# Kernel optimization log

Hardware: AMD Instinct MI355X
Metric: run time of the kernel (lower is better)

## Reference

```python
import jax, jax.numpy as jnp
import numpy as np

ID_LENGTH = 4   # number of identity images cached in the id bank
HEADS = 20      # SDXL attention heads at channel 1280
SA32 = 0.5


def setup_inputs() -> dict:
    key = jax.random.key(0)
    ks = jax.random.split(key, 7)
    B2, T, C = 8, 576, 1280            # 2*id_length images, 576 tokens each (768/32)^2
    S = ID_LENGTH * T                   # 2304 grouped sequence length
    hidden_states = jax.random.normal(ks[0], (B2, T, C), jnp.float32)
    # cal_attn_mask_xl: one random row pattern repeated, with each image's own
    # block forced True (sliced to the [:id_length*T, :id_length*T] write-mode mask)
    row_pat = jax.random.uniform(ks[1], (1, S)) < SA32
    mask = jnp.tile(row_pat, (S, 1))
    img = jnp.arange(S) // T
    mask = mask | (img[:, None] == img[None, :])
    w = lambda k: jax.random.normal(k, (C, C), jnp.float32) * 0.02
    return {
        "hidden_states": hidden_states,
        "mask": mask,
        "Wq": w(ks[2]), "Wk": w(ks[3]), "Wv": w(ks[4]), "Wo": w(ks[5]),
        "bo": jnp.zeros((C,), jnp.float32),
    }


def reference(hidden_states, mask, Wq, Wk, Wv, Wo, bo):
    # __call1__ path: regroup [2*id_length, T, C] -> [2, id_length*T, C]
    B2, T, C = hidden_states.shape
    hs = hidden_states.reshape(2, ID_LENGTH * T, C)
    hd = C // HEADS

    def split_heads(x):  # [2, S, C] -> [2, H, S, hd]
        return x.reshape(2, -1, HEADS, hd).transpose(0, 2, 1, 3)

    q = split_heads(hs @ Wq)
    k = split_heads(hs @ Wk)   # write mode: encoder_hidden_states == hidden_states
    v = split_heads(hs @ Wv)

    scores = jnp.einsum('bhqd,bhkd->bhqk', q, k) / jnp.sqrt(jnp.asarray(hd, q.dtype))
    scores = jnp.where(mask[None, None], scores, jnp.finfo(scores.dtype).min)
    attnw = jax.nn.softmax(scores, axis=-1)
    out = jnp.einsum('bhqk,bhkd->bhqd', attnw, v)
    out = out.transpose(0, 2, 1, 3).reshape(2, -1, C)
    out = out @ Wo + bo                 # attn.to_out[0]
    return out.reshape(B2, T, C)
```

## Files before the change

### kernel.cpp

```cpp
#include <hip/hip_runtime.h>
#include <hip/hip_bf16.h>
#include <stdint.h>
#include <math.h>

#define S_TOT 2304
#define C_DIM 1280
#define NHEAD 20
#define HD    64
#define M_TOT 4608
#define BH_STRIDE (S_TOT * HD)
#define SC_ROWS 2624
#define KC_STRIDE (SC_ROWS * 64)
#define LOG2E 1.44269504088896f
#define C_SC  (0.125f * LOG2E)
#define MFIX  12.0f
#define QBLK  192

typedef __attribute__((ext_vector_type(8))) short bf16x8;
typedef __attribute__((ext_vector_type(4))) float f32x4;

__device__ __forceinline__ short f2bf(float f) {
    union { float f; uint32_t u; } v; v.f = f;
    uint32_t r = v.u + 0x7FFFu + ((v.u >> 16) & 1u);
    return (short)(r >> 16);
}

__device__ __forceinline__ uint32_t pack2bf(float a, float b) {
    __hip_bfloat162 h = __float22bfloat162_rn(make_float2(a, b));
    union { __hip_bfloat162 h; uint32_t u; } cv; cv.h = h; return cv.u;
}

__device__ __forceinline__ f32x4 zero4() {
    f32x4 z; z[0] = 0.f; z[1] = 0.f; z[2] = 0.f; z[3] = 0.f; return z;
}

__device__ __forceinline__ void gload_lds16(const void* g, void* l) {
    __builtin_amdgcn_global_load_lds(
        (const __attribute__((address_space(1))) uint32_t*)g,
        (__attribute__((address_space(3))) uint32_t*)l, 16, 0, 0);
}

__global__ __launch_bounds__(256)
void prologue(const float* __restrict__ hs, short* __restrict__ hsb,
              const float* __restrict__ W0, const float* __restrict__ W1,
              const float* __restrict__ W2, const float* __restrict__ W3,
              short* __restrict__ T0, short* __restrict__ T1,
              short* __restrict__ T2, short* __restrict__ T3,
              const int* __restrict__ mask, int* __restrict__ hdr,
              int* __restrict__ destmap) {
    __shared__ float tile[32][33];
    __shared__ unsigned long long wbits[36];
    __shared__ int pp[36], dd[36], hb[9];

    const int bx = blockIdx.x;
    const int t = threadIdx.x;

    if (bx < 2880) {
        const int i = bx * 256 + t;
        const float4 v0 = reinterpret_cast<const float4*>(hs)[i * 2];
        const float4 v1 = reinterpret_cast<const float4*>(hs)[i * 2 + 1];
        bf16x8 o;
        o[0] = f2bf(v0.x); o[1] = f2bf(v0.y); o[2] = f2bf(v0.z); o[3] = f2bf(v0.w);
        o[4] = f2bf(v1.x); o[5] = f2bf(v1.y); o[6] = f2bf(v1.z); o[7] = f2bf(v1.w);
        reinterpret_cast<bf16x8*>(hsb)[i] = o;
    } else if (bx < 9280) {
        int id = bx - 2880;
        const int z = id / 1600; id -= z * 1600;
        const int by = id / 40, bxx = id - by * 40;
        const float* W; short* T;
        switch (z) {
            case 0:  W = W0; T = T0; break;
            case 1:  W = W1; T = T1; break;
            case 2:  W = W2; T = T2; break;
            default: W = W3; T = T3; break;
        }
        const int tx = t & 31, ty = t >> 5;
        const int k0 = by * 32, n0 = bxx * 32;
#pragma unroll
        for (int i = 0; i < 4; ++i)
            tile[ty + i * 8][tx] = W[(size_t)(k0 + ty + i * 8) * C_DIM + n0 + tx];
        __syncthreads();
#pragma unroll
        for (int i = 0; i < 4; ++i)
            T[(size_t)(n0 + ty + i * 8) * C_DIM + k0 + tx] = f2bf(tile[tx][ty + i * 8]);
    } else {
        for (int it = 0; it < 9; ++it) {
            const int k = it * 256 + t;
            const int src = (k < 1152) ? 1152 : 0;
            const bool pat = mask[(size_t)src * S_TOT + k] != 0;
            unsigned long long b = __ballot(pat);
            if ((t & 63) == 0) wbits[it * 4 + (t >> 6)] = b;
        }
        __syncthreads();
        if (t == 0) {
            int pcum = 0, dcum[4] = {0, 0, 0, 0};
            for (int wdx = 0; wdx < 36; ++wdx) {
                const int img = wdx / 9;
                const int pc = __popcll(wbits[wdx]);
                pp[wdx] = pcum; dd[wdx] = dcum[img];
                pcum += pc; dcum[img] += 64 - pc;
            }
            hb[0] = pcum;
            int base = (pcum + 63) & ~63;
            for (int i = 0; i < 4; ++i) {
                hb[1 + i] = base; hb[5 + i] = dcum[i];
                base += (dcum[i] + 63) & ~63;
            }
            for (int i = 0; i < 9; ++i) hdr[i] = hb[i];
        }
        __syncthreads();
        if (t < 36) {
            const unsigned long long w64 = wbits[t];
            const int img = t / 9;
            const int pbase = pp[t], dbase = hb[1 + img] + dd[t];
            int pc = 0, dc = 0;
            for (int b = 0; b < 64; ++b) {
                if ((w64 >> b) & 1) destmap[t * 64 + b] = pbase + (pc++);
                else                destmap[t * 64 + b] = dbase + (dc++);
            }
        }
    }
}

__global__ __launch_bounds__(256)
void zero_pads(const int* __restrict__ hdr, short* __restrict__ Kc,
               short* __restrict__ Vr) {
    const int bh = blockIdx.x;
    const int t = threadIdx.x;
    short* Kb = Kc + (size_t)bh * KC_STRIDE;
    short* Vb = Vr + (size_t)bh * KC_STRIDE;
    for (int seg = 0; seg < 5; ++seg) {
        const int cnt = (seg == 0) ? hdr[0] : hdr[4 + seg];
        const int sb  = (seg == 0) ? 0      : hdr[seg];
        const int s0 = sb + cnt;
        const int nrows = ((cnt + 63) & ~63) - cnt;
        for (int idx = t; idx < nrows * 64; idx += 256) {
            const int r = idx >> 6, d = idx & 63;
            Kb[(size_t)(s0 + r) * 64 + d] = 0;
            Vb[(size_t)(s0 + r) * 64 + d] = 0;
        }
    }
}

__global__ __launch_bounds__(256)
void transp_v(const short* __restrict__ Vr, short* __restrict__ Vc) {
    __shared__ short tile[64][72];
    const int bh = blockIdx.y;
    const int s0 = blockIdx.x * 64;
    const int t = threadIdx.x;
    const short* src = Vr + (size_t)bh * KC_STRIDE;
    short* dst = Vc + (size_t)bh * KC_STRIDE;

#pragma unroll
    for (int i = 0; i < 2; ++i) {
        const int e = (i * 256 + t) * 8;
        const int r = e >> 6, c = e & 63;
        bf16x8 v = *(const bf16x8*)(src + (size_t)(s0 + r) * 64 + c);
        *(bf16x8*)&tile[r][c] = v;
    }
    __syncthreads();
    const int d = t & 63, c0 = (t >> 6) * 16;
    short tmp[16];
#pragma unroll
    for (int j = 0; j < 16; ++j) tmp[j] = tile[c0 + j][d];
    *(bf16x8*)(dst + (size_t)d * SC_ROWS + s0 + c0) = *(const bf16x8*)tmp;
    *(bf16x8*)(dst + (size_t)d * SC_ROWS + s0 + c0 + 8) = *(const bf16x8*)(tmp + 8);
}

__global__ __launch_bounds__(256, 2)
void gemm_qkv3(const short* __restrict__ hsb,
               const short* __restrict__ Wtq, const short* __restrict__ Wtk,
               const short* __restrict__ Wtv, const int* __restrict__ destmap,
               short* __restrict__ Qb, short* __restrict__ Kc, short* __restrict__ Vr) {
    __shared__ short As[128 * 64];
    __shared__ short Bs[3 * 128 * 64];
    __shared__ int dm[128];

    const int bid = blockIdx.x;
    const int vid = (bid & 7) * 45 + (bid >> 3);
    const int n0 = (vid / 36) * 128, m0 = (vid % 36) * 128;
    const int t = threadIdx.x;
    const int lane = t & 63, w = t >> 6;
    const int g = lane >> 4, l15 = lane & 15;
    const int wm = w >> 1, wn = w & 1;

    if (t < 128) {
        const int s0 = (m0 >= S_TOT) ? m0 - S_TOT : m0;
        dm[t] = destmap[s0 + t];
    }

    f32x4 acc[3][4][4];
#pragma unroll
    for (int z = 0; z < 3; ++z)
#pragma unroll
        for (int mi = 0; mi < 4; ++mi)
#pragma unroll
            for (int ni = 0; ni < 4; ++ni) acc[z][mi][ni] = zero4();

    for (int k0 = 0; k0 < C_DIM; k0 += 64) {
        __syncthreads();
#pragma unroll
        for (int i = 0; i < 4; ++i) {
            const int F = i * 4096 + t * 16;
            const int row = F >> 7;
            const int colb = (F & 127) ^ ((row & 7) << 4);
            gload_lds16((const char*)hsb + ((size_t)(m0 + row) * C_DIM + k0) * 2 + colb,
                        (char*)As + F);
        }
#pragma unroll
        for (int z = 0; z < 3; ++z) {
            const short* Wt = (z == 0) ? Wtq : (z == 1) ? Wtk : Wtv;
#pragma unroll
            for (int i = 0; i < 4; ++i) {
                const int F = i * 4096 + t * 16;
                const int row = F >> 7;
                const int colb = (F & 127) ^ ((row & 7) << 4);
                gload_lds16((const char*)Wt + ((size_t)(n0 + row) * C_DIM + k0) * 2 + colb,
                            (char*)Bs + z * 16384 + F);
            }
        }
        __syncthreads();

#pragma unroll
        for (int ks = 0; ks < 2; ++ks) {
            const int kb = ks * 64 + g * 16;
            bf16x8 af[4];
#pragma unroll
            for (int mi = 0; mi < 4; ++mi) {
                const int row = wm * 64 + mi * 16 + l15;
                af[mi] = *(const bf16x8*)((const char*)As + row * 128 + (kb ^ ((row & 7) << 4)));
            }
#pragma unroll
            for (int z = 0; z < 3; ++z) {
                bf16x8 bfr[4];
#pragma unroll
                for (int ni = 0; ni < 4; ++ni) {
                    const int row = wn * 64 + ni * 16 + l15;
                    bfr[ni] = *(const bf16x8*)((const char*)Bs + z * 16384 + row * 128 + (kb ^ ((row & 7) << 4)));
                }
                __builtin_amdgcn_s_setprio(1);
#pragma unroll
                for (int mi = 0; mi < 4; ++mi)
#pragma unroll
                    for (int ni = 0; ni < 4; ++ni)
                        acc[z][mi][ni] = __builtin_amdgcn_mfma_f32_16x16x32_bf16(
                            af[mi], bfr[ni], acc[z][mi][ni], 0, 0, 0);
                __builtin_amdgcn_s_setprio(0);
            }
        }
    }

#pragma unroll
    for (int z = 0; z < 3; ++z)
#pragma unroll
        for (int mi = 0; mi < 4; ++mi)
#pragma unroll
            for (int ni = 0; ni < 4; ++ni)
#pragma unroll
                for (int r = 0; r < 4; ++r) {
                    const int m = m0 + wm * 64 + mi * 16 + g * 4 + r;
                    const int n = n0 + wn * 64 + ni * 16 + l15;
                    const int bg = (m >= S_TOT) ? 1 : 0;
                    const int s = m - bg * S_TOT;
                    const int h = n >> 6, d = n & 63;
                    const size_t bh = (size_t)(bg * NHEAD + h);
                    float aval = acc[z][mi][ni][r];
                    if (z == 0) aval *= C_SC;
                    const short v = f2bf(aval);
                    if (z == 0) {
                        Qb[bh * BH_STRIDE + (size_t)s * HD + d] = v;
                    } else {
                        const int sc = dm[m - m0];
                        short* dst = (z == 1) ? Kc : Vr;
                        dst[bh * (size_t)KC_STRIDE + (size_t)sc * 64 + d] = v;
                    }
                }
}

__device__ __forceinline__ void gemm_core(const short* __restrict__ A,
                                          const short* __restrict__ Wt,
                                          int m0, int n0,
                                          f32x4 acc[4][4],
                                          short* AsB, short* BsB) {
    const int t = threadIdx.x;
    const int lane = t & 63, w = t >> 6;
    const int g = lane >> 4, l15 = lane & 15;
    const int wm = w >> 1, wn = w & 1;

#pragma unroll
    for (int mi = 0; mi < 4; ++mi)
#pragma unroll
        for (int ni = 0; ni < 4; ++ni) acc[mi][ni] = zero4();

    auto stage = [&](int k0, int buf) {
#pragma unroll
        for (int i = 0; i < 4; ++i) {
            const int F = i * 4096 + t * 16;
            const int row = F >> 7;
            const int b = F & 127;
            const int colb = b ^ ((row & 7) << 4);
            gload_lds16((const char*)A + ((size_t)(m0 + row) * C_DIM + k0) * 2 + colb,
                        (char*)AsB + buf * 16384 + F);
            gload_lds16((const char*)Wt + ((size_t)(n0 + row) * C_DIM + k0) * 2 + colb,
                        (char*)BsB + buf * 16384 + F);
        }
    };

    stage(0, 0);
    asm volatile("s_waitcnt vmcnt(0)" ::: "memory");
    __builtin_amdgcn_s_barrier();
    __builtin_amdgcn_sched_barrier(0);

    int cur = 0;
    for (int k0 = 0; k0 < C_DIM; k0 += 64) {
        if (k0 + 64 < C_DIM) stage(k0 + 64, cur ^ 1);
        const char* Ac = (const char*)AsB + cur * 16384;
        const char* Bc = (const char*)BsB + cur * 16384;
#pragma unroll
        for (int ks = 0; ks < 2; ++ks) {
            const int kb = ks * 64 + g * 16;
            bf16x8 af[4], bfr[4];
#pragma unroll
            for (int mi = 0; mi < 4; ++mi) {
                const int row = wm * 64 + mi * 16 + l15;
                af[mi] = *(const bf16x8*)(Ac + row * 128 + (kb ^ ((row & 7) << 4)));
            }
#pragma unroll
            for (int ni = 0; ni < 4; ++ni) {
                const int row = wn * 64 + ni * 16 + l15;
                bfr[ni] = *(const bf16x8*)(Bc + row * 128 + (kb ^ ((row & 7) << 4)));
            }
            __builtin_amdgcn_s_setprio(1);
#pragma unroll
            for (int mi = 0; mi < 4; ++mi)
#pragma unroll
                for (int ni = 0; ni < 4; ++ni)
                    acc[mi][ni] = __builtin_amdgcn_mfma_f32_16x16x32_bf16(
                        af[mi], bfr[ni], acc[mi][ni], 0, 0, 0);
            __builtin_amdgcn_s_setprio(0);
        }
        asm volatile("s_waitcnt vmcnt(0)" ::: "memory");
        __builtin_amdgcn_s_barrier();
        __builtin_amdgcn_sched_barrier(0);
        cur ^= 1;
    }
}

__global__ __launch_bounds__(256)
void gemm_out(const short* __restrict__ Ab, const short* __restrict__ Wto,
              const float* __restrict__ bo, float* __restrict__ out) {
    __shared__ short As[2 * 128 * 64];
    __shared__ short Bs[2 * 128 * 64];
    const int bid = blockIdx.x;
    const int vid = (bid & 7) * 45 + (bid >> 3);
    const int n0 = (vid / 36) * 128, m0 = (vid % 36) * 128;

    f32x4 acc[4][4];
    gemm_core(Ab, Wto, m0, n0, acc, As, Bs);

    const int t = threadIdx.x;
    const int lane = t & 63, w = t >> 6, g = lane >> 4, l15 = lane & 15;
    const int wm = w >> 1, wn = w & 1;
#pragma unroll
    for (int mi = 0; mi < 4; ++mi)
#pragma unroll
        for (int ni = 0; ni < 4; ++ni) {
            const int n = n0 + wn * 64 + ni * 16 + l15;
            const float bias = bo[n];
#pragma unroll
            for (int r = 0; r < 4; ++r) {
                const int m = m0 + wm * 64 + mi * 16 + g * 4 + r;
                out[(size_t)m * C_DIM + n] = acc[mi][ni][r] + bias;
            }
        }
}

__global__ __launch_bounds__(768)
void attn_mfma(const short* __restrict__ Qb, const short* __restrict__ Kc,
               const short* __restrict__ Vc, const int* __restrict__ hdr,
               short* __restrict__ Ab) {
    __shared__ short Ks[3][4096];
    __shared__ short Vs[3][4096];
    __shared__ short Ps[QBLK * 64];

    const int t = threadIdx.x;
    const int lane = t & 63, w = t >> 6, g = lane >> 4, l15 = lane & 15;
    const int bid = blockIdx.x;
    const int vid = (bid & 7) * 60 + (bid >> 3);
    const int bh_i = vid / 12, qb = vid % 12;
    const int b = bh_i / NHEAD, h = bh_i % NHEAD;
    const int q0 = qb * QBLK;
    const size_t bh = (size_t)bh_i;
    const int qimg = qb / 3;

    const int cntp  = hdr[0];
    const int dbase = hdr[1 + qimg];
    const int cntd  = hdr[5 + qimg];
    const int ntp = (cntp + 63) >> 6, ntd = (cntd + 63) >> 6, nt = ntp + ntd;

    const short* Qp = Qb + bh * BH_STRIDE;
    const short* Kp = Kc + bh * (size_t)KC_STRIDE;
    const short* Vp = Vc + bh * (size_t)KC_STRIDE;

    bf16x8 qf[2];
    {
        const int row = q0 + w * 16 + l15;
        qf[0] = *(const bf16x8*)(Qp + (size_t)row * HD + g * 8);
        qf[1] = *(const bf16x8*)(Qp + (size_t)row * HD + 32 + g * 8);
    }

    bf16x8 onesv;
#pragma unroll
    for (int j = 0; j < 8; ++j) onesv[j] = (short)0x3F80;

    const f32x4 sinit = {-MFIX, -MFIX, -MFIX, -MFIX};
    f32x4 o_acc[4], lacc;
#pragma unroll
    for (int df = 0; df < 4; ++df) o_acc[df] = zero4();
    lacc = zero4();

    const int rowP = w * 16 + l15;
    const int swzP = (rowP & 7) << 4;
    const int ckbase = g * 4;

    auto tstart = [&](int tt) {
        return (tt < ntp) ? tt * 64 : dbase + (tt - ntp) * 64;
    };
    auto stage = [&](int start, int bufsel) {
        if (t < 512) {
            const int F = t * 16;
            const int row = F >> 7, bb = F & 127;
            const int colb = bb ^ ((row & 7) << 4);
            gload_lds16((const char*)Kp + (size_t)(start + row) * 128 + colb,
                        (char*)Ks[bufsel] + F);
            gload_lds16((const char*)Vp + (size_t)row * (SC_ROWS * 2) + start * 2 + colb,
                        (char*)Vs[bufsel] + F);
        }
    };

    stage(tstart(0), 0);
    if (nt > 1) stage(tstart(1), 1);
    asm volatile("s_waitcnt vmcnt(2)" ::: "memory");
    __builtin_amdgcn_s_barrier();
    __builtin_amdgcn_sched_barrier(0);

    for (int tt = 0; tt < nt; ++tt) {
        const int cur = tt % 3;
        if (tt + 2 < nt) stage(tstart(tt + 2), (tt + 2) % 3);
        const int lim = (tt < ntp) ? cntp - tt * 64 : cntd - (tt - ntp) * 64;

        f32x4 sacc[4];
#pragma unroll
        for (int nf = 0; nf < 4; ++nf) sacc[nf] = sinit;
        __builtin_amdgcn_s_setprio(1);
#pragma unroll
        for (int ks = 0; ks < 2; ++ks) {
            const int kb = ks * 64 + g * 16;
#pragma unroll
            for (int nf = 0; nf < 4; ++nf) {
                const int row = nf * 16 + l15;
                bf16x8 kf = *(const bf16x8*)((const char*)Ks[cur] + row * 128 + (kb ^ ((row & 7) << 4)));
                sacc[nf] = __builtin_amdgcn_mfma_f32_16x16x32_bf16(kf, qf[ks], sacc[nf], 0, 0, 0);
            }
        }
        __builtin_amdgcn_s_setprio(0);

        if (lim < 64) {
#pragma unroll
            for (int nf = 0; nf < 4; ++nf)
#pragma unroll
                for (int r = 0; r < 4; ++r)
                    if (nf * 16 + ckbase + r >= lim) sacc[nf][r] = -1e30f;
        }

#pragma unroll
        for (int nf = 0; nf < 4; ++nf) {
            uint2 u;
            u.x = pack2bf(__builtin_amdgcn_exp2f(sacc[nf][0]),
                          __builtin_amdgcn_exp2f(sacc[nf][1]));
            u.y = pack2bf(__builtin_amdgcn_exp2f(sacc[nf][2]),
                          __builtin_amdgcn_exp2f(sacc[nf][3]));
            *(uint2*)((char*)Ps + rowP * 128 + ((nf * 32 + g * 8) ^ swzP)) = u;
        }

        __builtin_amdgcn_s_setprio(1);
#pragma unroll
        for (int ks = 0; ks < 2; ++ks) {
            const int kb = ks * 64 + g * 16;
            bf16x8 pf = *(const bf16x8*)((const char*)Ps + rowP * 128 + (kb ^ swzP));
            lacc = __builtin_amdgcn_mfma_f32_16x16x32_bf16(onesv, pf, lacc, 0, 0, 0);
#pragma unroll
            for (int df = 0; df < 4; ++df) {
                const int rowV = df * 16 + l15;
                bf16x8 vf = *(const bf16x8*)((const char*)Vs[cur] + rowV * 128 + (kb ^ ((rowV & 7) << 4)));
                o_acc[df] = __builtin_amdgcn_mfma_f32_16x16x32_bf16(vf, pf, o_acc[df], 0, 0, 0);
            }
        }
        __builtin_amdgcn_s_setprio(0);

        asm volatile("s_waitcnt vmcnt(2)" ::: "memory");
        __builtin_amdgcn_s_barrier();
        __builtin_amdgcn_sched_barrier(0);
    }

    const float inv = 1.f / lacc[0];
    const int rowg = b * S_TOT + q0 + w * 16 + l15;
#pragma unroll
    for (int df = 0; df < 4; ++df) {
        uint2 u;
        u.x = pack2bf(o_acc[df][0] * inv, o_acc[df][1] * inv);
        u.y = pack2bf(o_acc[df][2] * inv, o_acc[df][3] * inv);
        *(uint2*)(Ab + (size_t)rowg * C_DIM + h * 64 + df * 16 + g * 4) = u;
    }
}

extern "C" void kernel_launch(void* const* d_in, const int* in_sizes, int n_in,
                              void* d_out, int out_size, void* d_ws, size_t ws_size,
                              hipStream_t stream)
{
    const float* hs   = (const float*)d_in[0];
    const int*   mask = (const int*)  d_in[1];
    const float* Wq   = (const float*)d_in[2];
    const float* Wk   = (const float*)d_in[3];
    const float* Wv   = (const float*)d_in[4];
    const float* Wo   = (const float*)d_in[5];
    const float* bo   = (const float*)d_in[6];
    float* out = (float*)d_out;

    char* ws = (char*)d_ws;
    const size_t mat_b = (size_t)M_TOT * C_DIM * 2;
    const size_t w_b   = (size_t)C_DIM * C_DIM * 2;
    const size_t kc_b  = (size_t)40 * KC_STRIDE * 2;

    short* hsb = (short*)ws;                 ws += mat_b;
    short* Wtq = (short*)ws;                 ws += w_b;
    short* Wtk = (short*)ws;                 ws += w_b;
    short* Wtv = (short*)ws;                 ws += w_b;
    short* Wto = (short*)ws;                 ws += w_b;
    short* Qb  = (short*)ws;                 ws += mat_b;
    short* Kc  = (short*)ws;                 ws += kc_b;
    short* Vr  = (short*)ws;                 ws += kc_b;
    short* Vc  = (short*)ws;                 ws += kc_b;
    short* Ab  = (short*)ws;                 ws += mat_b;
    int*   hdr = (int*)ws;                   ws += 64;
    int*   destmap = (int*)ws;               ws += S_TOT * 4;

    prologue<<<9281, 256, 0, stream>>>(hs, hsb, Wq, Wk, Wv, Wo,
                                       Wtq, Wtk, Wtv, Wto, mask, hdr, destmap);
    zero_pads<<<40, 256, 0, stream>>>(hdr, Kc, Vr);

    gemm_qkv3<<<360, 256, 0, stream>>>(
        hsb, Wtq, Wtk, Wtv, destmap, Qb, Kc, Vr);

    transp_v<<<dim3(SC_ROWS / 64, 40), 256, 0, stream>>>(Vr, Vc);

    attn_mfma<<<480, 768, 0, stream>>>(Qb, Kc, Vc, hdr, Ab);

    gemm_out<<<360, 256, 0, stream>>>(Ab, Wto, bo, out);
}
```

Baseline: 169.3 us.

## Give each attention wave three query fragments and widen output GEMM tile

The attention kernel drops from 12 waves per block to 4 waves, each handling 48 query rows in three 16-row fragments. Every K and V fragment read from LDS is reused across three MFMAs, which cuts LDS traffic per unit of compute at the cost of more registers and lower occupancy. The output GEMM moves to 256x128 tiles with 512 threads and 180 blocks, replacing the double-buffered async pipeline with single-buffered loads bracketed by __syncthreads. Losing the load/compute overlap in that GEMM may expose global memory latency.

```diff
diff --git a/kernel.cpp b/kernel.cpp
--- a/kernel.cpp
+++ b/kernel.cpp
@@ -277,45 +277,48 @@
                 }
 }
 
-__device__ __forceinline__ void gemm_core(const short* __restrict__ A,
-                                          const short* __restrict__ Wt,
-                                          int m0, int n0,
-                                          f32x4 acc[4][4],
-                                          short* AsB, short* BsB) {
+__global__ __launch_bounds__(512)
+void gemm_out(const short* __restrict__ Ab, const short* __restrict__ Wto,
+              const float* __restrict__ bo, float* __restrict__ out) {
+    __shared__ short As[256 * 64];
+    __shared__ short Bs[128 * 64];
+
+    const int bid = blockIdx.x;
+    const int xcd = bid & 7, idx = bid >> 3;
+    const int vid = (xcd < 4) ? xcd * 23 + idx : 92 + (xcd - 4) * 22 + idx;
+    const int m0 = (vid % 18) * 256, n0 = (vid / 18) * 128;
+
     const int t = threadIdx.x;
     const int lane = t & 63, w = t >> 6;
     const int g = lane >> 4, l15 = lane & 15;
     const int wm = w >> 1, wn = w & 1;
 
+    f32x4 acc[4][4];
 #pragma unroll
     for (int mi = 0; mi < 4; ++mi)
 #pragma unroll
         for (int ni = 0; ni < 4; ++ni) acc[mi][ni] = zero4();
 
-    auto stage = [&](int k0, int buf) {
+    for (int k0 = 0; k0 < C_DIM; k0 += 64) {
+        __syncthreads();
 #pragma unroll
         for (int i = 0; i < 4; ++i) {
-            const int F = i * 4096 + t * 16;
+            const int F = i * 8192 + t * 16;
             const int row = F >> 7;
-            const int b = F & 127;
-            const int colb = b ^ ((row & 7) << 4);
-            gload_lds16((const char*)A + ((size_t)(m0 + row) * C_DIM + k0) * 2 + colb,
-                        (char*)AsB + buf * 16384 + F);
-            gload_lds16((const char*)Wt + ((size_t)(n0 + row) * C_DIM + k0) * 2 + colb,
-                        (char*)BsB + buf * 16384 + F);
-        }
-    };
-
-    stage(0, 0);
-    asm volatile("s_waitcnt vmcnt(0)" ::: "memory");
-    __builtin_amdgcn_s_barrier();
-    __builtin_amdgcn_sched_barrier(0);
-
-    int cur = 0;
-    for (int k0 = 0; k0 < C_DIM; k0 += 64) {
-        if (k0 + 64 < C_DIM) stage(k0 + 64, cur ^ 1);
-        const char* Ac = (const char*)AsB + cur * 16384;
-        const char* Bc = (const char*)BsB + cur * 16384;
+            const int colb = (F & 127) ^ ((row & 7) << 4);
+            gload_lds16((const char*)Ab + ((size_t)(m0 + row) * C_DIM + k0) * 2 + colb,
+                        (char*)As + F);
+        }
+#pragma unroll
+        for (int i = 0; i < 2; ++i) {
+            const int F = i * 8192 + t * 16;
+            const int row = F >> 7;
+            const int colb = (F & 127) ^ ((row & 7) << 4);
+            gload_lds16((const char*)Wto + ((size_t)(n0 + row) * C_DIM + k0) * 2 + colb,
+                        (char*)Bs + F);
+        }
+        __syncthreads();
+
 #pragma unroll
         for (int ks = 0; ks < 2; ++ks) {
             const int kb = ks * 64 + g * 16;
@@ -323,12 +326,12 @@
 #pragma unroll
             for (int mi = 0; mi < 4; ++mi) {
                 const int row = wm * 64 + mi * 16 + l15;
-                af[mi] = *(const bf16x8*)(Ac + row * 128 + (kb ^ ((row & 7) << 4)));
+                af[mi] = *(const bf16x8*)((const char*)As + row * 128 + (kb ^ ((row & 7) << 4)));
             }
 #pragma unroll
             for (int ni = 0; ni < 4; ++ni) {
                 const int row = wn * 64 + ni * 16 + l15;
-                bfr[ni] = *(const bf16x8*)(Bc + row * 128 + (kb ^ ((row & 7) << 4)));
+                bfr[ni] = *(const bf16x8*)((const char*)Bs + row * 128 + (kb ^ ((row & 7) << 4)));
             }
             __builtin_amdgcn_s_setprio(1);
 #pragma unroll
@@ -339,28 +342,8 @@
                         af[mi], bfr[ni], acc[mi][ni], 0, 0, 0);
             __builtin_amdgcn_s_setprio(0);
         }
-        asm volatile("s_waitcnt vmcnt(0)" ::: "memory");
-        __builtin_amdgcn_s_barrier();
-        __builtin_amdgcn_sched_barrier(0);
-        cur ^= 1;
-    }
-}
-
-__global__ __launch_bounds__(256)
-void gemm_out(const short* __restrict__ Ab, const short* __restrict__ Wto,
-              const float* __restrict__ bo, float* __restrict__ out) {
-    __shared__ short As[2 * 128 * 64];
-    __shared__ short Bs[2 * 128 * 64];
-    const int bid = blockIdx.x;
-    const int vid = (bid & 7) * 45 + (bid >> 3);
-    const int n0 = (vid / 36) * 128, m0 = (vid % 36) * 128;
-
-    f32x4 acc[4][4];
-    gemm_core(Ab, Wto, m0, n0, acc, As, Bs);
-
-    const int t = threadIdx.x;
-    const int lane = t & 63, w = t >> 6, g = lane >> 4, l15 = lane & 15;
-    const int wm = w >> 1, wn = w & 1;
+    }
+
 #pragma unroll
     for (int mi = 0; mi < 4; ++mi)
 #pragma unroll
@@ -375,7 +358,7 @@
         }
 }
 
-__global__ __launch_bounds__(768)
+__global__ __launch_bounds__(256, 2)
 void attn_mfma(const short* __restrict__ Qb, const short* __restrict__ Kc,
                const short* __restrict__ Vc, const int* __restrict__ hdr,
                short* __restrict__ Ab) {
@@ -402,11 +385,12 @@
     const short* Kp = Kc + bh * (size_t)KC_STRIDE;
     const short* Vp = Vc + bh * (size_t)KC_STRIDE;
 
-    bf16x8 qf[2];
-    {
-        const int row = q0 + w * 16 + l15;
-        qf[0] = *(const bf16x8*)(Qp + (size_t)row * HD + g * 8);
-        qf[1] = *(const bf16x8*)(Qp + (size_t)row * HD + 32 + g * 8);
+    bf16x8 qf[3][2];
+#pragma unroll
+    for (int f = 0; f < 3; ++f) {
+        const int row = q0 + w * 48 + f * 16 + l15;
+        qf[f][0] = *(const bf16x8*)(Qp + (size_t)row * HD + g * 8);
+        qf[f][1] = *(const bf16x8*)(Qp + (size_t)row * HD + 32 + g * 8);
     }
 
     bf16x8 onesv;
@@ -414,21 +398,21 @@
     for (int j = 0; j < 8; ++j) onesv[j] = (short)0x3F80;
 
     const f32x4 sinit = {-MFIX, -MFIX, -MFIX, -MFIX};
-    f32x4 o_acc[4], lacc;
-#pragma unroll
-    for (int df = 0; df < 4; ++df) o_acc[df] = zero4();
-    lacc = zero4();
-
-    const int rowP = w * 16 + l15;
-    const int swzP = (rowP & 7) << 4;
-    const int ckbase = g * 4;
+    f32x4 o_acc[3][4], lacc[3];
+#pragma unroll
+    for (int f = 0; f < 3; ++f) {
+        lacc[f] = zero4();
+#pragma unroll
+        for (int df = 0; df < 4; ++df) o_acc[f][df] = zero4();
+    }
 
     auto tstart = [&](int tt) {
         return (tt < ntp) ? tt * 64 : dbase + (tt - ntp) * 64;
     };
     auto stage = [&](int start, int bufsel) {
-        if (t < 512) {
-            const int F = t * 16;
+#pragma unroll
+        for (int i = 0; i < 2; ++i) {
+            const int F = i * 4096 + t * 16;
             const int row = F >> 7, bb = F & 127;
             const int colb = bb ^ ((row & 7) << 4);
             gload_lds16((const char*)Kp + (size_t)(start + row) * 128 + colb,
@@ -440,18 +424,21 @@
 
     stage(tstart(0), 0);
     if (nt > 1) stage(tstart(1), 1);
-    asm volatile("s_waitcnt vmcnt(2)" ::: "memory");
+    asm volatile("s_waitcnt vmcnt(4)" ::: "memory");
     __builtin_amdgcn_s_barrier();
     __builtin_amdgcn_sched_barrier(0);
 
     for (int tt = 0; tt < nt; ++tt) {
         const int cur = tt % 3;
-        if (tt + 2 < nt) stage(tstart(tt + 2), (tt + 2) % 3);
+        const bool pre = (tt + 2 < nt);
+        if (pre) stage(tstart(tt + 2), (tt + 2) % 3);
         const int lim = (tt < ntp) ? cntp - tt * 64 : cntd - (tt - ntp) * 64;
 
-        f32x4 sacc[4];
-#pragma unroll
-        for (int nf = 0; nf < 4; ++nf) sacc[nf] = sinit;
+        f32x4 sacc[3][4];
+#pragma unroll
+        for (int f = 0; f < 3; ++f)
+#pragma unroll
+            for (int nf = 0; nf < 4; ++nf) sacc[f][nf] = sinit;
         __builtin_amdgcn_s_setprio(1);
 #pragma unroll
         for (int ks = 0; ks < 2; ++ks) {
@@ -460,57 +447,79 @@
             for (int nf = 0; nf < 4; ++nf) {
                 const int row = nf * 16 + l15;
                 bf16x8 kf = *(const bf16x8*)((const char*)Ks[cur] + row * 128 + (kb ^ ((row & 7) << 4)));
-                sacc[nf] = __builtin_amdgcn_mfma_f32_16x16x32_bf16(kf, qf[ks], sacc[nf], 0, 0, 0);
+#pragma unroll
+                for (int f = 0; f < 3; ++f)
+                    sacc[f][nf] = __builtin_amdgcn_mfma_f32_16x16x32_bf16(kf, qf[f][ks], sacc[f][nf], 0, 0, 0);
             }
         }
         __builtin_amdgcn_s_setprio(0);
 
         if (lim < 64) {
 #pragma unroll
-            for (int nf = 0; nf < 4; ++nf)
-#pragma unroll
-                for (int r = 0; r < 4; ++r)
-                    if (nf * 16 + ckbase + r >= lim) sacc[nf][r] = -1e30f;
-        }
-
-#pragma unroll
-        for (int nf = 0; nf < 4; ++nf) {
-            uint2 u;
-            u.x = pack2bf(__builtin_amdgcn_exp2f(sacc[nf][0]),
-                          __builtin_amdgcn_exp2f(sacc[nf][1]));
-            u.y = pack2bf(__builtin_amdgcn_exp2f(sacc[nf][2]),
-                          __builtin_amdgcn_exp2f(sacc[nf][3]));
-            *(uint2*)((char*)Ps + rowP * 128 + ((nf * 32 + g * 8) ^ swzP)) = u;
+            for (int f = 0; f < 3; ++f)
+#pragma unroll
+                for (int nf = 0; nf < 4; ++nf)
+#pragma unroll
+                    for (int r = 0; r < 4; ++r)
+                        if (nf * 16 + g * 4 + r >= lim) sacc[f][nf][r] = -1e30f;
+        }
+
+#pragma unroll
+        for (int f = 0; f < 3; ++f) {
+            const int rowP = w * 48 + f * 16 + l15;
+            const int swzP = (rowP & 7) << 4;
+#pragma unroll
+            for (int nf = 0; nf < 4; ++nf) {
+                uint2 u;
+                u.x = pack2bf(__builtin_amdgcn_exp2f(sacc[f][nf][0]),
+                              __builtin_amdgcn_exp2f(sacc[f][nf][1]));
+                u.y = pack2bf(__builtin_amdgcn_exp2f(sacc[f][nf][2]),
+                              __builtin_amdgcn_exp2f(sacc[f][nf][3]));
+                *(uint2*)((char*)Ps + rowP * 128 + ((nf * 32 + g * 8) ^ swzP)) = u;
+            }
         }
 
         __builtin_amdgcn_s_setprio(1);
 #pragma unroll
         for (int ks = 0; ks < 2; ++ks) {
             const int kb = ks * 64 + g * 16;
-            bf16x8 pf = *(const bf16x8*)((const char*)Ps + rowP * 128 + (kb ^ swzP));
-            lacc = __builtin_amdgcn_mfma_f32_16x16x32_bf16(onesv, pf, lacc, 0, 0, 0);
+            bf16x8 pf[3];
+#pragma unroll
+            for (int f = 0; f < 3; ++f) {
+                const int rowP = w * 48 + f * 16 + l15;
+                pf[f] = *(const bf16x8*)((const char*)Ps + rowP * 128 + (kb ^ ((rowP & 7) << 4)));
+            }
+#pragma unroll
+            for (int f = 0; f < 3; ++f)
+                lacc[f] = __builtin_amdgcn_mfma_f32_16x16x32_bf16(onesv, pf[f], lacc[f], 0, 0, 0);
 #pragma unroll
             for (int df = 0; df < 4; ++df) {
                 const int rowV = df * 16 + l15;
                 bf16x8 vf = *(const bf16x8*)((const char*)Vs[cur] + rowV * 128 + (kb ^ ((rowV & 7) << 4)));
-                o_acc[df] = __builtin_amdgcn_mfma_f32_16x16x32_bf16(vf, pf, o_acc[df], 0, 0, 0);
+#pragma unroll
+                for (int f = 0; f < 3; ++f)
+                    o_acc[f][df] = __builtin_amdgcn_mfma_f32_16x16x32_bf16(vf, pf[f], o_acc[f][df], 0, 0, 0);
             }
         }
         __builtin_amdgcn_s_setprio(0);
 
-        asm volatile("s_waitcnt vmcnt(2)" ::: "memory");
+        if (pre) { asm volatile("s_waitcnt vmcnt(4)" ::: "memory"); }
+        else     { asm volatile("s_waitcnt vmcnt(0)" ::: "memory"); }
         __builtin_amdgcn_s_barrier();
         __builtin_amdgcn_sched_barrier(0);
     }
 
-    const float inv = 1.f / lacc[0];
-    const int rowg = b * S_TOT + q0 + w * 16 + l15;
-#pragma unroll
-    for (int df = 0; df < 4; ++df) {
-        uint2 u;
-        u.x = pack2bf(o_acc[df][0] * inv, o_acc[df][1] * inv);
-        u.y = pack2bf(o_acc[df][2] * inv, o_acc[df][3] * inv);
-        *(uint2*)(Ab + (size_t)rowg * C_DIM + h * 64 + df * 16 + g * 4) = u;
+#pragma unroll
+    for (int f = 0; f < 3; ++f) {
+        const float inv = 1.f / lacc[f][0];
+        const int rowg = b * S_TOT + q0 + w * 48 + f * 16 + l15;
+#pragma unroll
+        for (int df = 0; df < 4; ++df) {
+            uint2 u;
+            u.x = pack2bf(o_acc[f][df][0] * inv, o_acc[f][df][1] * inv);
+            u.y = pack2bf(o_acc[f][df][2] * inv, o_acc[f][df][3] * inv);
+            *(uint2*)(Ab + (size_t)rowg * C_DIM + h * 64 + df * 16 + g * 4) = u;
+        }
     }
 }
 
@@ -554,7 +563,7 @@
 
     transp_v<<<dim3(SC_ROWS / 64, 40), 256, 0, stream>>>(Vr, Vc);
 
-    attn_mfma<<<480, 768, 0, stream>>>(Qb, Kc, Vc, hdr, Ab);
-
-    gemm_out<<<360, 256, 0, stream>>>(Ab, Wto, bo, out);
-}
+    attn_mfma<<<480, 256, 0, stream>>>(Qb, Kc, Vc, hdr, Ab);
+
+    gemm_out<<<180, 512, 0, stream>>>(Ab, Wto, bo, out);
+}
```

Result: slower. 180.7 us (+6.7%).
